# Kernel optimization log

Hardware: AMD Instinct MI355X
Metric: run time of the kernel (lower is better)

The kernel has to match this reference:

```python
import jax, jax.numpy as jnp
import numpy as np
from jax import lax

STRIDE = 4
RADII = [0.1, 0.2, 0.4, 0.8]   # initial radius 0.1, radius_scaling=2 per stage
NSAMPLE = 32
# per-stage conv channels [c_in(+3 for dp), c1, c2, c3]
CH = [[6, 64, 64, 128], [131, 128, 128, 256], [259, 256, 256, 512], [515, 512, 512, 1024]]


def _fps(xyz, npoint):
    """Furthest point sampling: xyz [B,N,3] -> idx [B,npoint] int32 (indices, no grad)."""
    xyz = lax.stop_gradient(xyz)
    B, N, _ = xyz.shape
    first = jnp.zeros((B,), jnp.int32)

    def step(carry, _):
        dists, last = carry
        lp = jnp.take_along_axis(xyz, last[:, None, None], axis=1)   # [B,1,3]
        d = jnp.sum((xyz - lp) ** 2, axis=-1)                        # [B,N]
        dists = jnp.minimum(dists, d)
        nxt = jnp.argmax(dists, axis=-1).astype(jnp.int32)
        return (dists, nxt), nxt

    init = (jnp.full((B, N), 1e10, xyz.dtype), first)
    _, rest = lax.scan(step, init, None, length=npoint - 1)          # [npoint-1, B]
    return jnp.concatenate([first[None], rest], axis=0).T            # [B, npoint]


def _ball_query(query, support, radius, nsample):
    """First nsample in-radius neighbor indices (lowest index first), padded with the
    first hit -- same semantics as the PointNet++ CUDA ball_query kernel."""
    query = lax.stop_gradient(query)
    support = lax.stop_gradient(support)
    N = support.shape[1]
    d2 = jnp.sum((query[:, :, None, :] - support[:, None, :, :]) ** 2, axis=-1)  # [B,Q,N]
    ar = jnp.arange(N, dtype=jnp.int32)
    key = jnp.where(d2 < radius * radius, ar[None, None, :], N)     # in-radius -> own index, else N
    neg_vals, order = lax.top_k(-key, nsample)                      # smallest indices first
    valid = (-neg_vals) < N
    return jnp.where(valid, order, order[..., :1])                  # [B,Q,nsample]


def _gather_pts(pts, idx):   # pts [B,N,3], idx [B,Q,S] -> [B,Q,S,3]
    return jax.vmap(lambda p, i: p[i])(pts, idx)


def _gather_feat(f, idx):    # f [B,C,N], idx [B,Q,S] -> [B,C,Q,S]
    return jax.vmap(lambda fb, i: fb[:, i])(f, idx)


def _local_aggr(query_xyz, support_xyz, feats, Ws, bs, radius, nsample):
    idx = _ball_query(query_xyz, support_xyz, radius, nsample)
    dp = _gather_pts(support_xyz, idx) - query_xyz[:, :, None, :]    # [B,Q,S,3] relative coords
    f = jnp.concatenate([jnp.transpose(dp, (0, 3, 1, 2)),            # [B,3,Q,S]
                         _gather_feat(feats, idx)], axis=1)          # [B,3+C,Q,S]
    for W, b in zip(Ws, bs):                                         # pointwise MLP over neighbors
        f = jax.nn.relu(jnp.einsum('oc,bcqs->boqs', W, f) + b[None, :, None, None])
    return jnp.max(f, axis=-1)                                       # max-pool over neighborhood -> [B,C_out,Q]


def _forward(xyz, Ws, bs):
    feats = jnp.transpose(xyz, (0, 2, 1))                            # features default to xyz^T: [B,3,N]
    support = xyz
    for k in range(4):                                               # 4 SA stages, stride 4 each
        npoint = support.shape[1] // STRIDE
        idx = _fps(support, npoint)
        query = jnp.take_along_axis(support, idx[:, :, None], axis=1)  # [B,npoint,3]
        feats = _local_aggr(query, support, feats, Ws[k], bs[k], RADII[k], NSAMPLE)
        support = query
    return feats                                                     # [B,1024,64]


def setup_inputs() -> dict:
    key = jax.random.key(0)
    ks = jax.random.split(key, 32)
    inp = {"xyz": jax.random.uniform(ks[0], (2, 16384, 3), jnp.float32)}
    i = 1
    for k in range(4):
        for l in range(3):
            cin, cout = CH[k][l], CH[k][l + 1]
            inp[f"w{k}{l}"] = jax.random.normal(ks[i], (cout, cin), jnp.float32) / np.sqrt(cin).astype(np.float32)
            i += 1
            inp[f"b{k}{l}"] = 0.01 * jax.random.normal(ks[i], (cout,), jnp.float32)
            i += 1
    return inp


def reference(xyz, w00, b00, w01, b01, w02, b02,
              w10, b10, w11, b11, w12, b12,
              w20, b20, w21, b21, w22, b22,
              w30, b30, w31, b31, w32, b32):
    Ws = [[w00, w01, w02], [w10, w11, w12], [w20, w21, w22], [w30, w31, w32]]
    bs = [[b00, b01, b02], [b10, b11, b12], [b20, b21, b22], [b30, b31, b32]]
    return _forward(xyz, Ws, bs)
```

## Files before the change

### kernel.cpp

```cpp
#include <hip/hip_runtime.h>
#include <cstdint>
#include <cstddef>

#define NBATCH 2
#define NSAMPLE 32

__global__ void xyzT_kernel(const float* __restrict__ xyz, float* __restrict__ xyzT, int N)
{
    int t = blockIdx.x * blockDim.x + threadIdx.x;
    int total = NBATCH * N;
    if (t >= total) return;
    int b = t / N, n = t - b * N;
    const float* p = xyz + ((size_t)b * N + n) * 3;
    float* o = xyzT + (size_t)b * 3 * N + n;
    o[0]            = p[0];
    o[(size_t)N]    = p[1];
    o[2 * (size_t)N] = p[2];
}

__global__ __launch_bounds__(1024)
__attribute__((amdgpu_waves_per_eu(4, 4)))
void fps_s0(const float* __restrict__ xyz, int npoint, float* __restrict__ query)
{
    const int N = 16384, BT = 1024;
    const int NW = 16;
    __shared__ float s_xy[2 * 16384];
    __shared__ unsigned long long s_wkey[2][NW];

    const int b = blockIdx.x;
    const int t = threadIdx.x;
    const int lane = t & 63;
    const int wid  = t >> 6;
    const float* xb = xyz + (size_t)b * N * 3;

    float pz[16], dd[16];
#pragma unroll
    for (int i = 0; i < 8; ++i)
#pragma unroll
        for (int j = 0; j < 2; ++j) {
            int p = 2 * (i * BT + t) + j;
            const float* pp = xb + (size_t)p * 3;
            s_xy[2 * p]     = pp[0];
            s_xy[2 * p + 1] = pp[1];
            pz[2 * i + j]   = pp[2];
            dd[2 * i + j]   = 1e10f;
        }

    float cx = xb[0], cy = xb[1], cz = xb[2];
    if (t == 0) {
        float* q = query + (size_t)b * npoint * 3;
        q[0] = cx; q[1] = cy; q[2] = cz;
    }

    for (int step = 1; step < npoint; ++step) {
        const int buf = step & 1;
        float bd = -1.0f;
        int bslot = 0;
#pragma unroll
        for (int i = 0; i < 8; ++i) {
            const float4 v = *(const float4*)&s_xy[4 * (i * BT + t)];
            {
                float dx = v.x - cx, dy = v.y - cy, dz = pz[2 * i] - cz;
                float d = __fmul_rn(dx, dx);
                d = __fadd_rn(d, __fmul_rn(dy, dy));
                d = __fadd_rn(d, __fmul_rn(dz, dz));
                float nd = fminf(dd[2 * i], d);
                dd[2 * i] = nd;
                bool g = nd > bd;
                bd    = g ? nd : bd;
                bslot = g ? (2 * i) : bslot;
            }
            {
                float dx = v.z - cx, dy = v.w - cy, dz = pz[2 * i + 1] - cz;
                float d = __fmul_rn(dx, dx);
                d = __fadd_rn(d, __fmul_rn(dy, dy));
                d = __fadd_rn(d, __fmul_rn(dz, dz));
                float nd = fminf(dd[2 * i + 1], d);
                dd[2 * i + 1] = nd;
                bool g = nd > bd;
                bd    = g ? nd : bd;
                bslot = g ? (2 * i + 1) : bslot;
            }
        }
        int bidx = 2 * ((bslot >> 1) * BT + t) + (bslot & 1);
        unsigned long long key =
            ((unsigned long long)__float_as_uint(bd) << 32) | (unsigned int)(~bidx);
#pragma unroll
        for (int m = 1; m < 64; m <<= 1) {
            unsigned long long o = __shfl_xor(key, m);
            key = (o > key) ? o : key;
        }
        if (lane == 0) s_wkey[buf][wid] = key;
        __syncthreads();
        unsigned long long v[NW];
#pragma unroll
        for (int w = 0; w < NW; ++w) v[w] = s_wkey[buf][w];
#pragma unroll
        for (int s = NW / 2; s > 0; s >>= 1)
#pragma unroll
            for (int w = 0; w < NW / 2; ++w)
                if (w < s) v[w] = (v[w + s] > v[w]) ? v[w + s] : v[w];
        unsigned int widx = ~(unsigned int)v[0];
        const float* wp = xb + (size_t)widx * 3;
        cx = wp[0]; cy = wp[1]; cz = wp[2];
        if (t == 0) {
            float* q = query + ((size_t)b * npoint + step) * 3;
            q[0] = cx; q[1] = cy; q[2] = cz;
        }
    }
}

template<int PPT, int BT, int WPE>
__global__ __launch_bounds__(BT)
__attribute__((amdgpu_waves_per_eu(WPE, WPE)))
void fps_gen(const float* __restrict__ xyz, int npoint, float* __restrict__ query)
{
    const int N = PPT * BT;
    constexpr int NW = BT / 64;
    __shared__ float4 s_p[PPT * BT];
    __shared__ unsigned long long s_wkey[2][NW];

    const int b = blockIdx.x;
    const int t = threadIdx.x;
    const int lane = t & 63;
    const int wid  = t >> 6;
    const float* xb = xyz + (size_t)b * N * 3;

    float dd[PPT];
#pragma unroll
    for (int i = 0; i < PPT; ++i) {
        int p = i * BT + t;
        const float* pp = xb + (size_t)p * 3;
        s_p[p] = make_float4(pp[0], pp[1], pp[2], 0.0f);
        dd[i] = 1e10f;
    }

    float cx = xb[0], cy = xb[1], cz = xb[2];
    if (t == 0) {
        float* q = query + (size_t)b * npoint * 3;
        q[0] = cx; q[1] = cy; q[2] = cz;
    }

    for (int step = 1; step < npoint; ++step) {
        const int buf = step & 1;
        float bd = -1.0f;
        int bslot = 0;
#pragma unroll
        for (int i = 0; i < PPT; ++i) {
            const float4 v = s_p[i * BT + t];
            float dx = v.x - cx, dy = v.y - cy, dz = v.z - cz;
            float d = __fmul_rn(dx, dx);
            d = __fadd_rn(d, __fmul_rn(dy, dy));
            d = __fadd_rn(d, __fmul_rn(dz, dz));
            float nd = fminf(dd[i], d);
            dd[i] = nd;
            bool g = nd > bd;
            bd    = g ? nd : bd;
            bslot = g ? i : bslot;
        }
        int bidx = bslot * BT + t;
        unsigned long long key =
            ((unsigned long long)__float_as_uint(bd) << 32) | (unsigned int)(~bidx);
#pragma unroll
        for (int m = 1; m < 64; m <<= 1) {
            unsigned long long o = __shfl_xor(key, m);
            key = (o > key) ? o : key;
        }
        if (lane == 0) s_wkey[buf][wid] = key;
        __syncthreads();
        unsigned long long v[NW];
#pragma unroll
        for (int w = 0; w < NW; ++w) v[w] = s_wkey[buf][w];
#pragma unroll
        for (int s = NW / 2; s > 0; s >>= 1)
#pragma unroll
            for (int w = 0; w < NW / 2; ++w)
                if (w < s) v[w] = (v[w + s] > v[w]) ? v[w + s] : v[w];
        unsigned int widx = ~(unsigned int)v[0];
        const float* wp = xb + (size_t)widx * 3;
        cx = wp[0]; cy = wp[1]; cz = wp[2];
        if (t == 0) {
            float* q = query + ((size_t)b * npoint + step) * 3;
            q[0] = cx; q[1] = cy; q[2] = cz;
        }
    }
}

__global__ void ballquery_kernel(const float* __restrict__ support,
                                 const float* __restrict__ query,
                                 int N, int Q, float r2,
                                 int* __restrict__ nbr)
{
    int gw   = (blockIdx.x * blockDim.x + threadIdx.x) >> 6;
    int lane = threadIdx.x & 63;
    if (gw >= NBATCH * Q) return;
    int b = gw / Q;
    int q = gw - b * Q;

    const float* sb = support + (size_t)b * N * 3;
    const float* qp = query + ((size_t)b * Q + q) * 3;
    float qx = qp[0], qy = qp[1], qz = qp[2];
    int* out = nbr + ((size_t)b * Q + q) * NSAMPLE;

    int cnt = 0, first = 0;
    for (int base = 0; base < N; base += 64) {
        int j = base + lane;
        float dx = __fsub_rn(sb[j * 3 + 0], qx);
        float dy = __fsub_rn(sb[j * 3 + 1], qy);
        float dz = __fsub_rn(sb[j * 3 + 2], qz);
        float d2 = __fmul_rn(dx, dx);
        d2 = __fadd_rn(d2, __fmul_rn(dy, dy));
        d2 = __fadd_rn(d2, __fmul_rn(dz, dz));
        bool inr = d2 < r2;
        unsigned long long mask = __ballot(inr);
        if (mask) {
            if (cnt == 0) first = base + (int)__builtin_ctzll(mask);
            if (inr) {
                int pos = cnt + (int)__popcll(mask & ((1ull << lane) - 1ull));
                if (pos < NSAMPLE) out[pos] = j;
            }
            cnt += (int)__popcll(mask);
            if (cnt >= NSAMPLE) break;
        }
    }
    for (int pos = cnt + lane; pos < NSAMPLE; pos += 64) out[pos] = first;
}

__global__ void gather_kernel(const float* __restrict__ support,
                              const float* __restrict__ query,
                              const int* __restrict__ nbr,
                              const float* __restrict__ feats,
                              int N, int Q, int C, int b,
                              float* __restrict__ F0)
{
    int n = blockIdx.x * blockDim.x + threadIdx.x;
    int Nn = Q * NSAMPLE;
    if (n >= Nn) return;
    int q = n >> 5, s = n & 31;
    int j = nbr[((size_t)b * Q + q) * NSAMPLE + s];
    const float* sp = support + ((size_t)b * N + j) * 3;
    const float* qp = query + ((size_t)b * Q + q) * 3;
    size_t NnS = (size_t)Nn;
    F0[n]           = sp[0] - qp[0];
    F0[NnS + n]     = sp[1] - qp[1];
    F0[2 * NnS + n] = sp[2] - qp[2];
    const float* fb = feats + (size_t)b * C * N;
    float* Fo = F0 + 3 * NnS + n;
    for (int c = 0; c < C; ++c) Fo[(size_t)c * NnS] = fb[(size_t)c * N + j];
}

template<bool POOL>
__global__ __launch_bounds__(256)
void gemm_relu(const float* __restrict__ W, const float* __restrict__ bias,
               const float* __restrict__ F, float* __restrict__ Out,
               int M, int K, int Nn, int b)
{
    __shared__ float Ws[16][64];
    __shared__ float Fs[16][68];

    const int n0 = blockIdx.x * 64;
    const int m0 = blockIdx.y * 64;
    const int tid = threadIdx.x;
    const int tx = tid & 15, ty = tid >> 4;

    float acc[4][4] = {};

    const int wm = tid >> 2;
    const int wk = (tid & 3) * 4;
    const int fk = tid >> 4;
    const int fn = (tid & 15) * 4;

    for (int k0 = 0; k0 < K; k0 += 16) {
#pragma unroll
        for (int j = 0; j < 4; ++j) {
            int kk = wk + j;
            int kg = k0 + kk;
            Ws[kk][wm] = (kg < K) ? W[(size_t)(m0 + wm) * K + kg] : 0.0f;
        }
        {
            int kg = k0 + fk;
            float4 v = make_float4(0.f, 0.f, 0.f, 0.f);
            if (kg < K) v = *(const float4*)(F + (size_t)kg * Nn + n0 + fn);
            *(float4*)&Fs[fk][fn] = v;
        }
        __syncthreads();
#pragma unroll
        for (int kk = 0; kk < 16; ++kk) {
            float av[4], bv[4];
            *(float4*)av = *(const float4*)&Ws[kk][ty * 4];
            *(float4*)bv = *(const float4*)&Fs[kk][tx * 4];
#pragma unroll
            for (int i = 0; i < 4; ++i)
#pragma unroll
                for (int j = 0; j < 4; ++j)
                    acc[i][j] = fmaf(av[i], bv[j], acc[i][j]);
        }
        __syncthreads();
    }

    if constexpr (!POOL) {
#pragma unroll
        for (int i = 0; i < 4; ++i) {
            int m = m0 + ty * 4 + i;
            float bvs = bias[m];
            float4 r;
            r.x = fmaxf(acc[i][0] + bvs, 0.0f);
            r.y = fmaxf(acc[i][1] + bvs, 0.0f);
            r.z = fmaxf(acc[i][2] + bvs, 0.0f);
            r.w = fmaxf(acc[i][3] + bvs, 0.0f);
            *(float4*)(Out + (size_t)m * Nn + n0 + tx * 4) = r;
        }
    } else {
        __shared__ float Cs[64][65];
#pragma unroll
        for (int i = 0; i < 4; ++i) {
            int mr = ty * 4 + i;
            float bvs = bias[m0 + mr];
#pragma unroll
            for (int j = 0; j < 4; ++j)
                Cs[mr][tx * 4 + j] = fmaxf(acc[i][j] + bvs, 0.0f);
        }
        __syncthreads();
        if (tid < 128) {
            int r = tid >> 1, g = tid & 1;
            float mx = Cs[r][g * 32];
            for (int c = 1; c < 32; ++c) mx = fmaxf(mx, Cs[r][g * 32 + c]);
            int Qn = Nn >> 5;
            Out[((size_t)b * M + m0 + r) * Qn + (n0 >> 5) + g] = mx;
        }
    }
}

extern "C" void kernel_launch(void* const* d_in, const int* in_sizes, int n_in,
                              void* d_out, int out_size, void* d_ws, size_t ws_size,
                              hipStream_t stream)
{
    (void)in_sizes; (void)n_in; (void)out_size; (void)ws_size;
    const float* xyz = (const float*)d_in[0];
    const float* W[4][3]; const float* Bi[4][3];
    for (int k = 0; k < 4; ++k)
        for (int l = 0; l < 3; ++l) {
            W[k][l]  = (const float*)d_in[1 + k * 6 + l * 2];
            Bi[k][l] = (const float*)d_in[2 + k * 6 + l * 2];
        }
    float* out = (float*)d_out;

    uintptr_t cur = (uintptr_t)d_ws;
    auto alloc = [&](size_t bytes) -> void* {
        void* p = (void*)cur;
        cur += (bytes + 255) & ~(size_t)255;
        return p;
    };
    float* xyzT = (float*)alloc((size_t)NBATCH * 3 * 16384 * sizeof(float));
    float* qA   = (float*)alloc((size_t)NBATCH * 4096 * 3 * sizeof(float));
    float* qB   = (float*)alloc((size_t)NBATCH * 4096 * 3 * sizeof(float));
    int*   nbr  = (int*)  alloc((size_t)NBATCH * 4096 * NSAMPLE * sizeof(int));
    float* f0   = (float*)alloc((size_t)NBATCH * 128 * 4096 * sizeof(float));
    float* f1   = (float*)alloc((size_t)NBATCH * 256 * 1024 * sizeof(float));
    float* f2   = (float*)alloc((size_t)NBATCH * 512 * 256 * sizeof(float));
    float* X = (float*)alloc((size_t)8388608 * sizeof(float));
    float* Y = (float*)alloc((size_t)8388608 * sizeof(float));

    xyzT_kernel<<<(NBATCH * 16384 + 255) / 256, 256, 0, stream>>>(xyz, xyzT, 16384);

    struct StageP { int N, Q, Cprev, c1, c2, c3; double r; };
    const StageP st[4] = {
        {16384, 4096,   3,   64,  64,  128, 0.1},
        { 4096, 1024, 128,  128, 128,  256, 0.2},
        { 1024,  256, 256,  256, 256,  512, 0.4},
        {  256,   64, 512,  512, 512, 1024, 0.8},
    };
    const float* support   = xyz;
    const float* featsPrev = xyzT;
    float* qbuf[2]     = {qA, qB};
    float* featsOut[4] = {f0, f1, f2, out};

    for (int k = 0; k < 4; ++k) {
        const StageP& s = st[k];
        float* qcur = qbuf[k & 1];
        if      (k == 0) fps_s0<<<NBATCH, 1024, 0, stream>>>(support, s.Q, qcur);
        else if (k == 1) fps_gen<8, 512, 2><<<NBATCH, 512, 0, stream>>>(support, s.Q, qcur);
        else if (k == 2) fps_gen<2, 512, 2><<<NBATCH, 512, 0, stream>>>(support, s.Q, qcur);
        else             fps_gen<1, 256, 1><<<NBATCH, 256, 0, stream>>>(support, s.Q, qcur);

        float r2 = (float)(s.r * s.r);
        ballquery_kernel<<<(NBATCH * s.Q) / 4, 256, 0, stream>>>(support, qcur, s.N, s.Q, r2, nbr);

        int K0 = 3 + s.Cprev;
        int Nn = s.Q * NSAMPLE;
        for (int b = 0; b < NBATCH; ++b) {
            gather_kernel<<<(Nn + 255) / 256, 256, 0, stream>>>(
                support, qcur, nbr, featsPrev, s.N, s.Q, s.Cprev, b, X);
            gemm_relu<false><<<dim3(Nn / 64, s.c1 / 64, 1), 256, 0, stream>>>(
                W[k][0], Bi[k][0], X, Y, s.c1, K0, Nn, 0);
            gemm_relu<false><<<dim3(Nn / 64, s.c2 / 64, 1), 256, 0, stream>>>(
                W[k][1], Bi[k][1], Y, X, s.c2, s.c1, Nn, 0);
            gemm_relu<true><<<dim3(Nn / 64, s.c3 / 64, 1), 256, 0, stream>>>(
                W[k][2], Bi[k][2], X, featsOut[k], s.c3, s.c2, Nn, b);
        }
        support   = qcur;
        featsPrev = featsOut[k];
    }
}
```

Measured before the change: 10.28 ms.

## Accelerate FPS with Morton-sorted point clusters and bounding-sphere pruning

Adds a cluster_build kernel that Morton-sorts the points into 64-point clusters and stores each cluster's centroid and bounding radius. A new fps_cluster kernel uses these bounds each step to skip distance updates for clusters that cannot change, keeping one max key per cluster. It is used for the first two stages instead of the dense FPS kernels. The cost is a bitonic sort and extra setup launches, plus per-step cluster tests and wave reductions per active cluster that could cost more when few clusters are pruned.

```diff
diff --git a/kernel.cpp b/kernel.cpp
--- a/kernel.cpp
+++ b/kernel.cpp
@@ -18,33 +18,158 @@
     o[2 * (size_t)N] = p[2];
 }
 
-__global__ __launch_bounds__(1024)
-__attribute__((amdgpu_waves_per_eu(4, 4)))
-void fps_s0(const float* __restrict__ xyz, int npoint, float* __restrict__ query)
-{
-    const int N = 16384, BT = 1024;
-    const int NW = 16;
-    __shared__ float s_xy[2 * 16384];
-    __shared__ unsigned long long s_wkey[2][NW];
+__device__ inline unsigned p1b2(unsigned x)
+{
+    x &= 0x3FFu;
+    x = (x | (x << 16)) & 0x030000FFu;
+    x = (x | (x << 8))  & 0x0300F00Fu;
+    x = (x | (x << 4))  & 0x030C30C3u;
+    x = (x | (x << 2))  & 0x09249249u;
+    return x;
+}
+
+template<int N>
+__global__ __launch_bounds__(512)
+void cluster_build(const float* __restrict__ xyz,
+                   float* __restrict__ gx, float* __restrict__ gy,
+                   float* __restrict__ gz, unsigned* __restrict__ gidx,
+                   float4* __restrict__ gstats)
+{
+    constexpr int BT = 512, G = N / 64;
+    __shared__ unsigned long long sk[N];
+    __shared__ float s_red[8][6];
+    __shared__ float s_bb[6];
 
     const int b = blockIdx.x;
     const int t = threadIdx.x;
-    const int lane = t & 63;
-    const int wid  = t >> 6;
+    const int lane = t & 63, w = t >> 6;
     const float* xb = xyz + (size_t)b * N * 3;
-
-    float pz[16], dd[16];
-#pragma unroll
-    for (int i = 0; i < 8; ++i)
-#pragma unroll
-        for (int j = 0; j < 2; ++j) {
-            int p = 2 * (i * BT + t) + j;
-            const float* pp = xb + (size_t)p * 3;
-            s_xy[2 * p]     = pp[0];
-            s_xy[2 * p + 1] = pp[1];
-            pz[2 * i + j]   = pp[2];
-            dd[2 * i + j]   = 1e10f;
-        }
+    gx += (size_t)b * N; gy += (size_t)b * N; gz += (size_t)b * N;
+    gidx += (size_t)b * N; gstats += (size_t)b * G;
+
+    float mnx = 1e30f, mny = 1e30f, mnz = 1e30f;
+    float mxx = -1e30f, mxy = -1e30f, mxz = -1e30f;
+    for (int p = t; p < N; p += BT) {
+        float x = xb[3 * p], y = xb[3 * p + 1], z = xb[3 * p + 2];
+        mnx = fminf(mnx, x); mxx = fmaxf(mxx, x);
+        mny = fminf(mny, y); mxy = fmaxf(mxy, y);
+        mnz = fminf(mnz, z); mxz = fmaxf(mxz, z);
+    }
+#pragma unroll
+    for (int m = 1; m < 64; m <<= 1) {
+        mnx = fminf(mnx, __shfl_xor(mnx, m)); mxx = fmaxf(mxx, __shfl_xor(mxx, m));
+        mny = fminf(mny, __shfl_xor(mny, m)); mxy = fmaxf(mxy, __shfl_xor(mxy, m));
+        mnz = fminf(mnz, __shfl_xor(mnz, m)); mxz = fmaxf(mxz, __shfl_xor(mxz, m));
+    }
+    if (lane == 0) {
+        s_red[w][0] = mnx; s_red[w][1] = mny; s_red[w][2] = mnz;
+        s_red[w][3] = mxx; s_red[w][4] = mxy; s_red[w][5] = mxz;
+    }
+    __syncthreads();
+    if (t == 0) {
+        for (int c = 0; c < 3; ++c) {
+            float mn = s_red[0][c], mx = s_red[0][3 + c];
+            for (int i = 1; i < 8; ++i) {
+                mn = fminf(mn, s_red[i][c]);
+                mx = fmaxf(mx, s_red[i][3 + c]);
+            }
+            s_bb[c] = mn; s_bb[3 + c] = mx;
+        }
+    }
+    __syncthreads();
+    const float bx = s_bb[0], by = s_bb[1], bz = s_bb[2];
+    const float sx = 1024.0f / fmaxf(s_bb[3] - bx, 1e-9f);
+    const float sy = 1024.0f / fmaxf(s_bb[4] - by, 1e-9f);
+    const float sz = 1024.0f / fmaxf(s_bb[5] - bz, 1e-9f);
+
+    for (int p = t; p < N; p += BT) {
+        unsigned cx = min(1023, (int)((xb[3 * p] - bx) * sx));
+        unsigned cy = min(1023, (int)((xb[3 * p + 1] - by) * sy));
+        unsigned cz = min(1023, (int)((xb[3 * p + 2] - bz) * sz));
+        unsigned m = (p1b2(cz) << 2) | (p1b2(cy) << 1) | p1b2(cx);
+        sk[p] = ((unsigned long long)m << 14) | (unsigned)p;
+    }
+    __syncthreads();
+
+    for (int k = 2; k <= N; k <<= 1) {
+        for (int jj = k >> 1; jj > 0; jj >>= 1) {
+            for (int q = t; q < N / 2; q += BT) {
+                int i = ((q & ~(jj - 1)) << 1) | (q & (jj - 1));
+                int pr = i | jj;
+                unsigned long long a = sk[i], c = sk[pr];
+                bool asc = ((i & k) == 0);
+                if ((a > c) == asc) { sk[i] = c; sk[pr] = a; }
+            }
+            __syncthreads();
+        }
+    }
+
+    for (int s = t; s < N; s += BT) {
+        unsigned p = (unsigned)(sk[s] & 0x3FFFu);
+        gidx[s] = p;
+        gx[s] = xb[3 * p];
+        gy[s] = xb[3 * p + 1];
+        gz[s] = xb[3 * p + 2];
+    }
+    __threadfence_block();
+    __syncthreads();
+
+    for (int c = w; c < G; c += 8) {
+        int slot = c * 64 + lane;
+        float x = gx[slot], y = gy[slot], z = gz[slot];
+        float sxx = x, syy = y, szz = z;
+#pragma unroll
+        for (int m = 1; m < 64; m <<= 1) {
+            sxx += __shfl_xor(sxx, m);
+            syy += __shfl_xor(syy, m);
+            szz += __shfl_xor(szz, m);
+        }
+        float ccx = sxx * (1.0f / 64.0f), ccy = syy * (1.0f / 64.0f), ccz = szz * (1.0f / 64.0f);
+        float dx = x - ccx, dy = y - ccy, dz = z - ccz;
+        float d2 = dx * dx + dy * dy + dz * dz;
+#pragma unroll
+        for (int m = 1; m < 64; m <<= 1) d2 = fmaxf(d2, __shfl_xor(d2, m));
+        if (lane == 0)
+            gstats[c] = make_float4(ccx, ccy, ccz, sqrtf(d2) * 1.00001f + 1e-6f);
+    }
+}
+
+template<int N, int BT>
+__global__ __launch_bounds__(BT)
+void fps_cluster(const float* __restrict__ xyz,
+                 const float* __restrict__ gx, const float* __restrict__ gy,
+                 const float* __restrict__ gz, const unsigned* __restrict__ gidx,
+                 const float4* __restrict__ gstats,
+                 int npoint, float* __restrict__ query)
+{
+    constexpr int G = N / 64, NW = BT / 64, OWN = G / NW;
+    __shared__ float s_xy[2 * N];
+    __shared__ unsigned long long s_key[2][G];
+    __shared__ float4 s_cst[G];
+
+    const int b = blockIdx.x;
+    const int t = threadIdx.x;
+    const int lane = t & 63, w = t >> 6;
+    const float* xb = xyz + (size_t)b * N * 3;
+    gx += (size_t)b * N; gy += (size_t)b * N; gz += (size_t)b * N;
+    gidx += (size_t)b * N;
+    gstats += (size_t)b * G;
+
+    float zr[OWN], dd[OWN];
+    unsigned pidx[OWN];
+#pragma unroll
+    for (int j = 0; j < OWN; ++j) {
+        int g = j * NW + w;
+        int s = g * 64 + lane;
+        s_xy[2 * s]     = gx[s];
+        s_xy[2 * s + 1] = gy[s];
+        zr[j]   = gz[s];
+        pidx[j] = gidx[s];
+        dd[j]   = 1e10f;
+    }
+    unsigned long long mykey = ((unsigned long long)__float_as_uint(1e10f) << 32);
+    for (int i = t; i < G; i += BT) s_cst[i] = gstats[i];
+    __syncthreads();
 
     float cx = xb[0], cy = xb[1], cz = xb[2];
     if (t == 0) {
@@ -54,53 +179,51 @@
 
     for (int step = 1; step < npoint; ++step) {
         const int buf = step & 1;
-        float bd = -1.0f;
-        int bslot = 0;
-#pragma unroll
-        for (int i = 0; i < 8; ++i) {
-            const float4 v = *(const float4*)&s_xy[4 * (i * BT + t)];
-            {
-                float dx = v.x - cx, dy = v.y - cy, dz = pz[2 * i] - cz;
+        bool f = false;
+        if (lane < OWN) {
+            const float4 cs = s_cst[lane * NW + w];
+            float dx = cs.x - cx, dy = cs.y - cy, dz = cs.z - cz;
+            float d2c = dx * dx + dy * dy + dz * dz;
+            float mdd = __uint_as_float((unsigned)(mykey >> 32));
+            float Dlb = sqrtf(d2c) * 0.99999f - cs.w;
+            f = !(Dlb > 0.0f && Dlb * Dlb * 0.99998f >= mdd);
+        }
+        unsigned long long fm = __ballot(f);
+#pragma unroll
+        for (int j = 0; j < OWN; ++j) {
+            if ((fm >> j) & 1ull) {
+                int s = (j * NW + w) * 64 + lane;
+                const float2 xy = *(const float2*)&s_xy[2 * s];
+                float dx = xy.x - cx, dy = xy.y - cy, dz = zr[j] - cz;
                 float d = __fmul_rn(dx, dx);
                 d = __fadd_rn(d, __fmul_rn(dy, dy));
                 d = __fadd_rn(d, __fmul_rn(dz, dz));
-                float nd = fminf(dd[2 * i], d);
-                dd[2 * i] = nd;
-                bool g = nd > bd;
-                bd    = g ? nd : bd;
-                bslot = g ? (2 * i) : bslot;
+                float nd = fminf(dd[j], d);
+                dd[j] = nd;
+                unsigned long long k =
+                    ((unsigned long long)__float_as_uint(nd) << 32) | (unsigned)(~pidx[j]);
+#pragma unroll
+                for (int m = 1; m < 64; m <<= 1) {
+                    unsigned long long o = __shfl_xor(k, m);
+                    k = (o > k) ? o : k;
+                }
+                if (lane == j) mykey = k;
             }
-            {
-                float dx = v.z - cx, dy = v.w - cy, dz = pz[2 * i + 1] - cz;
-                float d = __fmul_rn(dx, dx);
-                d = __fadd_rn(d, __fmul_rn(dy, dy));
-                d = __fadd_rn(d, __fmul_rn(dz, dz));
-                float nd = fminf(dd[2 * i + 1], d);
-                dd[2 * i + 1] = nd;
-                bool g = nd > bd;
-                bd    = g ? nd : bd;
-                bslot = g ? (2 * i + 1) : bslot;
-            }
-        }
-        int bidx = 2 * ((bslot >> 1) * BT + t) + (bslot & 1);
-        unsigned long long key =
-            ((unsigned long long)__float_as_uint(bd) << 32) | (unsigned int)(~bidx);
+        }
+        if (lane < OWN) s_key[buf][lane * NW + w] = mykey;
+        __syncthreads();
+        unsigned long long bk = s_key[buf][lane];
+#pragma unroll
+        for (int k2 = 1; k2 < G / 64; ++k2) {
+            unsigned long long o = s_key[buf][lane + 64 * k2];
+            bk = (o > bk) ? o : bk;
+        }
 #pragma unroll
         for (int m = 1; m < 64; m <<= 1) {
-            unsigned long long o = __shfl_xor(key, m);
-            key = (o > key) ? o : key;
-        }
-        if (lane == 0) s_wkey[buf][wid] = key;
-        __syncthreads();
-        unsigned long long v[NW];
-#pragma unroll
-        for (int w = 0; w < NW; ++w) v[w] = s_wkey[buf][w];
-#pragma unroll
-        for (int s = NW / 2; s > 0; s >>= 1)
-#pragma unroll
-            for (int w = 0; w < NW / 2; ++w)
-                if (w < s) v[w] = (v[w + s] > v[w]) ? v[w + s] : v[w];
-        unsigned int widx = ~(unsigned int)v[0];
+            unsigned long long o = __shfl_xor(bk, m);
+            bk = (o > bk) ? o : bk;
+        }
+        unsigned widx = ~(unsigned)bk;
         const float* wp = xb + (size_t)widx * 3;
         cx = wp[0]; cy = wp[1]; cz = wp[2];
         if (t == 0) {
@@ -360,6 +483,16 @@
     float* f2   = (float*)alloc((size_t)NBATCH * 512 * 256 * sizeof(float));
     float* X = (float*)alloc((size_t)8388608 * sizeof(float));
     float* Y = (float*)alloc((size_t)8388608 * sizeof(float));
+    float*    c0x = (float*)   alloc((size_t)NBATCH * 16384 * sizeof(float));
+    float*    c0y = (float*)   alloc((size_t)NBATCH * 16384 * sizeof(float));
+    float*    c0z = (float*)   alloc((size_t)NBATCH * 16384 * sizeof(float));
+    unsigned* c0i = (unsigned*)alloc((size_t)NBATCH * 16384 * sizeof(unsigned));
+    float4*   c0s = (float4*)  alloc((size_t)NBATCH * 256 * sizeof(float4));
+    float*    c1x = (float*)   alloc((size_t)NBATCH * 4096 * sizeof(float));
+    float*    c1y = (float*)   alloc((size_t)NBATCH * 4096 * sizeof(float));
+    float*    c1z = (float*)   alloc((size_t)NBATCH * 4096 * sizeof(float));
+    unsigned* c1i = (unsigned*)alloc((size_t)NBATCH * 4096 * sizeof(unsigned));
+    float4*   c1s = (float4*)  alloc((size_t)NBATCH * 64 * sizeof(float4));
 
     xyzT_kernel<<<(NBATCH * 16384 + 255) / 256, 256, 0, stream>>>(xyz, xyzT, 16384);
 
@@ -378,10 +511,19 @@
     for (int k = 0; k < 4; ++k) {
         const StageP& s = st[k];
         float* qcur = qbuf[k & 1];
-        if      (k == 0) fps_s0<<<NBATCH, 1024, 0, stream>>>(support, s.Q, qcur);
-        else if (k == 1) fps_gen<8, 512, 2><<<NBATCH, 512, 0, stream>>>(support, s.Q, qcur);
-        else if (k == 2) fps_gen<2, 512, 2><<<NBATCH, 512, 0, stream>>>(support, s.Q, qcur);
-        else             fps_gen<1, 256, 1><<<NBATCH, 256, 0, stream>>>(support, s.Q, qcur);
+        if (k == 0) {
+            cluster_build<16384><<<NBATCH, 512, 0, stream>>>(support, c0x, c0y, c0z, c0i, c0s);
+            fps_cluster<16384, 1024><<<NBATCH, 1024, 0, stream>>>(
+                support, c0x, c0y, c0z, c0i, c0s, s.Q, qcur);
+        } else if (k == 1) {
+            cluster_build<4096><<<NBATCH, 512, 0, stream>>>(support, c1x, c1y, c1z, c1i, c1s);
+            fps_cluster<4096, 512><<<NBATCH, 512, 0, stream>>>(
+                support, c1x, c1y, c1z, c1i, c1s, s.Q, qcur);
+        } else if (k == 2) {
+            fps_gen<2, 512, 2><<<NBATCH, 512, 0, stream>>>(support, s.Q, qcur);
+        } else {
+            fps_gen<1, 256, 1><<<NBATCH, 256, 0, stream>>>(support, s.Q, qcur);
+        }
 
         float r2 = (float)(s.r * s.r);
         ballquery_kernel<<<(NBATCH * s.Q) / 4, 256, 0, stream>>>(support, qcur, s.N, s.Q, r2, nbr);
```

New measurement: 15.30 ms. 1.49x slower.
